# Performance work log

Hardware: AMD Instinct MI355X
Metric: run time of the kernel (lower is better)

The kernel has to match this reference:

```python
import jax, jax.numpy as jnp
import numpy as np

Nx, Nu, Ny, Np, H = 2, 1, 2, 8, 32
Nz = Np * (Nx + Nu)  # 24
B, T = 4096, 256
F, V, Delta = 0.1, 1.0, 1.0  # ps.squeeze(), volume, sample time
ymean = jnp.array([0.5, 0.5], jnp.float32)
ystd = jnp.array([0.3, 0.2], jnp.float32)
umean = jnp.array([1.0], jnp.float32)
ustd = jnp.array([0.5], jnp.float32)


def fnn(x, params):
    # dense layers: tanh hidden, linear output
    for W, b in params[:-1]:
        x = jnp.tanh(x @ W + b)
    W, b = params[-1]
    return x @ W + b


def fxzu(x, z, u, p1, p2, p3):
    # dCa/dt = F*(Caf-Ca)/V - r1 ; dCb/dt = -F*Cb/V + r1 - 3*r2 + r3
    Castd, Cbstd = ystd[0:1], ystd[1:2]
    r1 = fnn(x[:, 0:1], p1) * Castd
    r2 = fnn(x[:, 1:2], p2) * Cbstd
    r3 = fnn(z, p3) * Cbstd
    xs = x * ystd + ymean
    us = u * ustd + umean
    Ca, Cb, Caf = xs[:, 0:1], xs[:, 1:2], us[:, 0:1]
    dCa = F * (Caf - Ca) / V - r1
    dCb = -F * Cb / V + r1 - 3.0 * r2 + r3
    return jnp.concatenate([dCa, dCb], axis=-1) / ystd


def interp(yseq):
    # (B,(Np+1)*Nx) -> (B, Np*Nx): midpoints of consecutive Nx-blocks
    b = yseq.shape[0]
    y = yseq.reshape(b, Np + 1, Nx)
    return (0.5 * (y[:, :-1] + y[:, 1:])).reshape(b, Np * Nx)


def run(useq, xz0, p1, p2, p3):
    def step(xz, u):
        x, z = xz[:, :Nx], xz[:, Nx:]
        xpseq, upseq = z[:, :Np * Nx], z[:, Np * Nx:]
        k1 = fxzu(x, z, u, p1, p2, p3)
        z23 = jnp.concatenate([interp(jnp.concatenate([xpseq, x], -1)), upseq], -1)
        k2 = fxzu(x + Delta * k1 / 2, z23, u, p1, p2, p3)
        k3 = fxzu(x + Delta * k2 / 2, z23, u, p1, p2, p3)
        z4 = jnp.concatenate([xpseq[:, Nx:], x, upseq], -1)
        k4 = fxzu(x + Delta * k3, z4, u, p1, p2, p3)
        xplus = x + (Delta / 6.0) * (k1 + 2 * k2 + 2 * k3 + k4)
        zplus = jnp.concatenate([xpseq[:, Nx:], x, upseq[:, Nu:], u], -1)
        return jnp.concatenate([xplus, zplus], -1), x  # output is pre-update x
    _, ys = jax.lax.scan(step, xz0, jnp.swapaxes(useq, 0, 1))
    return jnp.swapaxes(ys, 0, 1)  # (B, T, Ny)


def setup_inputs() -> dict:
    key = jax.random.key(0)
    ks = jax.random.split(key, 12)
    inp = {
        'useq': jax.random.normal(ks[0], (B, T, Nu), jnp.float32),
        'xz0': jax.random.normal(ks[1], (B, Nx + Nz), jnp.float32),
    }
    dims = {'r1': [1, H, H, 1], 'r2': [1, H, H, 1], 'r3': [Nz, H, H, 1]}
    i = 2
    for name, ds in dims.items():
        for l, (din, dout) in enumerate(zip(ds[:-1], ds[1:])):
            inp[f'{name}W{l}'] = jax.random.normal(ks[i], (din, dout), jnp.float32) / np.sqrt(din).astype(np.float32)
            inp[f'{name}b{l}'] = jnp.zeros((dout,), jnp.float32)
            i += 1
    return inp


def reference(useq, xz0, r1W0, r1b0, r1W1, r1b1, r1W2, r1b2,
              r2W0, r2b0, r2W1, r2b1, r2W2, r2b2,
              r3W0, r3b0, r3W1, r3b1, r3W2, r3b2):
    p1 = [(r1W0, r1b0), (r1W1, r1b1), (r1W2, r1b2)]
    p2 = [(r2W0, r2b0), (r2W1, r2b1), (r2W2, r2b2)]
    p3 = [(r3W0, r3b0), (r3W1, r3b1), (r3W2, r3b2)]
    return run(useq, xz0, p1, p2, p3)
```

## Files before the change

kernel.cpp:

```cpp
#include <hip/hip_runtime.h>

#define DEVINL static __device__ __forceinline__
#define CFENCE() asm volatile("" ::: "memory")
#define PIN(x) asm volatile("" : "+v"(x))

typedef float v2f __attribute__((ext_vector_type(2)));

DEVINL v2f mk2(float a, float b) { v2f r; r.x = a; r.y = b; return r; }
DEVINL v2f pkfma(v2f a, v2f b, v2f c) { return __builtin_elementwise_fma(a, b, c); }

constexpr float KE = 2.885390081777927f;

#if __has_builtin(__builtin_amdgcn_exp2f)
DEVINL float exp2_fast(float x) { return __builtin_amdgcn_exp2f(x); }
#else
DEVINL float exp2_fast(float x) { return __expf(x * 0.6931471805599453f); }
#endif

DEVINL float tanh_pre(float t) {
  float e = exp2_fast(t);
  return 1.0f - 2.0f * __builtin_amdgcn_rcpf(e + 1.0f);
}

template <int CTRL>
DEVINL float dpp_add(float v) {
  int t = __builtin_amdgcn_update_dpp(0, __float_as_int(v), CTRL, 0xF, 0xF, true);
  return v + __int_as_float(t);
}
DEVINL float halves_psum(float v) {
  v = dpp_add<0xB1>(v);
  v = dpp_add<0x4E>(v);
  v = dpp_add<0x141>(v);
  v = dpp_add<0x140>(v);
  return v;
}
DEVINL float rlane(float v, int l) {
  return __int_as_float(__builtin_amdgcn_readlane(__float_as_int(v), l));
}

DEVINL float dot32(const float* hrow, const v2f* W, float bias) {
  const float4* hp = (const float4*)hrow;
  v2f a0 = mk2(bias, 0.f), a1 = mk2(0.f, 0.f);
  v2f a2 = mk2(0.f, 0.f), a3 = mk2(0.f, 0.f);
#pragma unroll
  for (int q = 0; q < 8; q += 2) {
    float4 x = hp[q], y = hp[q + 1];
    a0 = pkfma(mk2(x.x, x.y), W[2 * q + 0], a0);
    a1 = pkfma(mk2(x.z, x.w), W[2 * q + 1], a1);
    a2 = pkfma(mk2(y.x, y.y), W[2 * q + 2], a2);
    a3 = pkfma(mk2(y.z, y.w), W[2 * q + 3], a3);
  }
  v2f s = (a0 + a1) + (a2 + a3);
  return s.x + s.y;
}
DEVINL float pdot16(const float* hrow, const v2f* W) {
  const float4* hp = (const float4*)hrow;
  v2f a0 = mk2(0.f, 0.f), a1 = mk2(0.f, 0.f);
  float4 x = hp[0], y = hp[1];
  a0 = pkfma(mk2(x.x, x.y), W[0], a0);
  a1 = pkfma(mk2(x.z, x.w), W[1], a1);
  a0 = pkfma(mk2(y.x, y.y), W[2], a0);
  a1 = pkfma(mk2(y.z, y.w), W[3], a1);
  x = hp[2]; y = hp[3];
  a0 = pkfma(mk2(x.x, x.y), W[4], a0);
  a1 = pkfma(mk2(x.z, x.w), W[5], a1);
  a0 = pkfma(mk2(y.x, y.y), W[6], a0);
  a1 = pkfma(mk2(y.z, y.w), W[7], a1);
  v2f s = a0 + a1;
  return s.x + s.y;
}

constexpr int TT = 256;

__global__ __attribute__((amdgpu_flat_work_group_size(64, 64)))
__attribute__((amdgpu_waves_per_eu(4, 4))) void reac_kernel(
    const float* __restrict__ useq,
    const float* __restrict__ xz0,
    const float* __restrict__ r1W0, const float* __restrict__ r1b0,
    const float* __restrict__ r1W1, const float* __restrict__ r1b1,
    const float* __restrict__ r1W2, const float* __restrict__ r1b2,
    const float* __restrict__ r2W0, const float* __restrict__ r2b0,
    const float* __restrict__ r2W1, const float* __restrict__ r2b1,
    const float* __restrict__ r2W2, const float* __restrict__ r2b2,
    const float* __restrict__ r3W0, const float* __restrict__ r3b0,
    const float* __restrict__ r3W1, const float* __restrict__ r3b1,
    const float* __restrict__ r3W2, const float* __restrict__ r3b2,
    float2* __restrict__ out)
{
  const int lane = threadIdx.x;
  const int j = lane & 31;
  const bool hi = lane >= 32;
  const int b = blockIdx.x;
  const int xaddr = ((lane ^ 32) << 2);

  auto xchg = [&](float v) -> float {
    return __int_as_float(__builtin_amdgcn_ds_bpermute(xaddr, __float_as_int(v)));
  };

  const float* W0p = hi ? r2W0 : r1W0;
  const float* B0p = hi ? r2b0 : r1b0;
  const float* W1p = hi ? r2W1 : r1W1;
  const float* B1p = hi ? r2b1 : r1b1;
  const float* W2p = hi ? r2W2 : r1W2;
  const float sc = hi ? 0.2f : 0.3f;
  float w0K = W0p[j] * KE, b0K = B0p[j] * KE;
  float b1K = B1p[j] * KE;
  float w2sc = W2p[j] * sc;

  v2f W1v[16];
#pragma unroll
  for (int k = 0; k < 16; ++k)
    W1v[k] = mk2(W1p[(2 * k) * 32 + j] * KE, W1p[(2 * k + 1) * 32 + j] * KE);

  v2f W0Cv[12];
#pragma unroll
  for (int m = 0; m < 12; ++m) {
    int r = (hi && m >= 1 && m <= 7) ? (2 * m - 2) : (2 * m);
    v2f w = mk2(r3W0[r * 32 + j] * KE, r3W0[(r + 1) * 32 + j] * KE);
    if (hi && m == 0) w = mk2(0.f, 0.f);
    W0Cv[m] = w;
  }
  v2f WXv = mk2(r3W0[14 * 32 + j] * KE, r3W0[15 * 32 + j] * KE);

  const int kbase = hi ? 16 : 0;
  v2f W1Cv[8];
#pragma unroll
  for (int k = 0; k < 8; ++k)
    W1Cv[k] = mk2(r3W1[(kbase + 2 * k) * 32 + j] * KE,
                  r3W1[(kbase + 2 * k + 1) * 32 + j] * KE);
  float b0CK = r3b0[j] * KE, b1CK = r3b1[j] * KE;
  float w2C02 = r3W2[j] * 0.2f;

  PIN(w0K); PIN(b0K); PIN(b1K); PIN(w2sc);
  PIN(b0CK); PIN(b1CK); PIN(w2C02); PIN(WXv);
#pragma unroll
  for (int k = 0; k < 16; ++k) PIN(W1v[k]);
#pragma unroll
  for (int m = 0; m < 12; ++m) PIN(W0Cv[m]);
#pragma unroll
  for (int k = 0; k < 8; ++k) PIN(W1Cv[k]);

  const float b2sA = r1b2[0] * 0.3f;
  const float b2sB = r2b2[0] * 0.2f;
  const float b2Cs = r3b2[0] * 0.2f - 0.05f;

  __shared__ __align__(16) float zs[24];
  __shared__ __align__(16) float h12[2][32];
  __shared__ __align__(16) float hR3[3][32];

  float x0 = xz0[b * 26 + 0];
  float x1 = xz0[b * 26 + 1];
  if (!hi && j < 24) zs[j] = xz0[b * 26 + 2 + j];
  CFENCE();

  auto r3_l0 = [&](v2f& aaO, v2f& abO) {
    const float4* zp4 = (const float4*)&zs[0];
    float4 z0v = zp4[0], z1v = zp4[1], z2v = zp4[2], z3v = zp4[3];
    float4 u0v = zp4[4], u1v = zp4[5];
    v2f aa = mk2(b0CK, 0.f), ab = mk2(0.f, 0.f);
    aa = pkfma(mk2(z0v.x, z0v.y), W0Cv[0], aa);
    ab = pkfma(mk2(z0v.z, z0v.w), W0Cv[1], ab);
    aa = pkfma(mk2(z1v.x, z1v.y), W0Cv[2], aa);
    ab = pkfma(mk2(z1v.z, z1v.w), W0Cv[3], ab);
    aa = pkfma(mk2(z2v.x, z2v.y), W0Cv[4], aa);
    ab = pkfma(mk2(z2v.z, z2v.w), W0Cv[5], ab);
    aa = pkfma(mk2(z3v.x, z3v.y), W0Cv[6], aa);
    ab = pkfma(mk2(z3v.z, z3v.w), W0Cv[7], ab);
    aa = pkfma(mk2(u0v.x, u0v.y), W0Cv[8], aa);
    ab = pkfma(mk2(u0v.z, u0v.w), W0Cv[9], ab);
    aa = pkfma(mk2(u1v.x, u1v.y), W0Cv[10], aa);
    ab = pkfma(mk2(u1v.z, u1v.w), W0Cv[11], ab);
    aaO = aa; abO = ab;
  };
  auto rc1_eval = [&]() -> float {
    float p0 = pdot16(&hR3[0][kbase], W1Cv);
    float o0 = p0 + xchg(p0) + b1CK;
    float v = halves_psum(tanh_pre(o0) * w2C02);
    return (rlane(v, 15) + rlane(v, 31)) + b2Cs;
  };

  auto net_pre = [&](float sxv, float syv) -> float {
    float sv = hi ? syv : sxv;
    return tanh_pre(fmaf(sv, w0K, b0K));
  };
  auto net_post = [&](float sxv, float syv, float rc_m05, float CafF,
                      float& kx, float& ky) {
    float a = dot32(&h12[hi][0], W1v, b1K);
    float v = halves_psum(tanh_pre(a) * w2sc);
    float ra = (rlane(v, 15) + rlane(v, 31)) + b2sA;
    float rb = (rlane(v, 47) + rlane(v, 63)) + b2sB;
    float dCa = fmaf(-0.03f, sxv, CafF) - ra;
    float dCb = fmaf(-0.02f, syv, fmaf(-3.0f, rb, ra) + rc_m05);
    kx = dCa * (1.0f / 0.3f);
    ky = dCb * (1.0f / 0.2f);
  };

  v2f aa4, ab4;
  float Az;
  r3_l0(aa4, ab4);
  {
    v2f s = aa4 + ab4;
    Az = s.x + s.y;
    float h0 = tanh_pre(Az);
    CFENCE();
    if (!hi) hR3[0][j] = h0;
    CFENCE();
  }
  float rc1 = rc1_eval();

  float u = useq[b * TT];

  for (int t = 0; t < TT; ++t) {
    int tn = (t < TT - 1) ? (t + 1) : t;
    float u_nxt = useq[b * TT + tn];
    float CafF = fmaf(u, 0.05f, 0.05f);

    if (lane == 0) out[b * TT + t] = make_float2(x0, x1);

    ab4 = pkfma(mk2(x0, x1), WXv, ab4);
    v2f s4v = aa4 + ab4;
    float A4 = s4v.x + s4v.y;
    float Apart = xchg(hi ? A4 : Az);
    float targ = hi ? A4 : (0.5f * (Az + Apart));
    float hh = tanh_pre(targ);
    float h1 = net_pre(x0, x1);
    CFENCE();
    hR3[1 + hi][j] = hh;
    h12[hi][j] = h1;
    CFENCE();
    float p1 = pdot16(&hR3[1][kbase], W1Cv);
    float p2 = pdot16(&hR3[2][kbase], W1Cv);
    float o1 = p1 + xchg(p1) + b1CK;
    float o2 = p2 + xchg(p2) + b1CK;
    float vv = halves_psum(tanh_pre(hi ? o2 : o1) * w2C02);
    float rc23 = (rlane(vv, 15) + rlane(vv, 31)) + b2Cs;
    float rc4  = (rlane(vv, 47) + rlane(vv, 63)) + b2Cs;
    float kx1, ky1;
    net_post(x0, x1, rc1, CafF, kx1, ky1);
    float sx2 = fmaf(kx1, 0.5f, x0), sy2 = fmaf(ky1, 0.5f, x1);
    float h2 = net_pre(sx2, sy2);
    CFENCE();
    h12[hi][j] = h2;
    CFENCE();
    float kx2, ky2;
    net_post(sx2, sy2, rc23, CafF, kx2, ky2);
    {
      int src = (j < 14) ? (j + 2) : ((j < 23) ? (j + 1) : 0);
      float zread = zs[src];
      float znew = (j == 14) ? x0 : ((j == 15) ? x1 : ((j == 23) ? u : zread));
      if ((!hi) && (j < 24)) zs[j] = znew;
    }
    CFENCE();
    r3_l0(aa4, ab4);
    {
      v2f sv2 = aa4 + ab4;
      Az = sv2.x + sv2.y;
      float h0n = tanh_pre(Az);
      if (!hi) hR3[0][j] = h0n;
    }
    float sx3 = fmaf(kx2, 0.5f, x0), sy3 = fmaf(ky2, 0.5f, x1);
    float h3 = net_pre(sx3, sy3);
    CFENCE();
    h12[hi][j] = h3;
    CFENCE();
    float kx3, ky3;
    net_post(sx3, sy3, rc23, CafF, kx3, ky3);
    rc1 = rc1_eval();
    float sx4 = x0 + kx3, sy4 = x1 + ky3;
    float h4 = net_pre(sx4, sy4);
    CFENCE();
    h12[hi][j] = h4;
    CFENCE();
    float kx4, ky4;
    net_post(sx4, sy4, rc4, CafF, kx4, ky4);
    x0 += (kx1 + 2.0f * (kx2 + kx3) + kx4) * (1.0f / 6.0f);
    x1 += (ky1 + 2.0f * (ky2 + ky3) + ky4) * (1.0f / 6.0f);
    u = u_nxt;
    CFENCE();
  }
}

extern "C" void kernel_launch(void* const* d_in, const int* in_sizes, int n_in,
                              void* d_out, int out_size, void* d_ws, size_t ws_size,
                              hipStream_t stream) {
  const float* p[20];
  for (int i = 0; i < 20; ++i) p[i] = (const float*)d_in[i];
  reac_kernel<<<dim3(4096), dim3(64), 0, stream>>>(
      p[0], p[1], p[2], p[3], p[4], p[5], p[6], p[7], p[8], p[9], p[10],
      p[11], p[12], p[13], p[14], p[15], p[16], p[17], p[18], p[19],
      (float2*)d_out);
}
```

Before: 844.7 us.

## Move per-lane weights from registers to shared LDS and pack four waves per block

Per-lane weight vectors for the hidden layers used to be pinned in VGPRs. They now live in a shared-memory table written once by the first wave and read by all four waves of a 256-thread block, so each block handles four batch elements. The aim is to cut register pressure and the redundant weight loads so more waves fit per SIMD, which should hide the latency of this serial scan loop. The cost is extra LDS reads on every dot product inside the time loop, which may contend with the existing LDS traffic for activations.

```diff
diff --git a/kernel.cpp b/kernel.cpp
--- a/kernel.cpp
+++ b/kernel.cpp
@@ -2,7 +2,6 @@
 
 #define DEVINL static __device__ __forceinline__
 #define CFENCE() asm volatile("" ::: "memory")
-#define PIN(x) asm volatile("" : "+v"(x))
 
 typedef float v2f __attribute__((ext_vector_type(2)));
 
@@ -27,53 +26,20 @@
   int t = __builtin_amdgcn_update_dpp(0, __float_as_int(v), CTRL, 0xF, 0xF, true);
   return v + __int_as_float(t);
 }
-DEVINL float halves_psum(float v) {
+DEVINL float rlane(float v, int l) {
+  return __int_as_float(__builtin_amdgcn_readlane(__float_as_int(v), l));
+}
+DEVINL float psum4(float v) {
   v = dpp_add<0xB1>(v);
   v = dpp_add<0x4E>(v);
   v = dpp_add<0x141>(v);
   v = dpp_add<0x140>(v);
   return v;
 }
-DEVINL float rlane(float v, int l) {
-  return __int_as_float(__builtin_amdgcn_readlane(__float_as_int(v), l));
-}
-
-DEVINL float dot32(const float* hrow, const v2f* W, float bias) {
-  const float4* hp = (const float4*)hrow;
-  v2f a0 = mk2(bias, 0.f), a1 = mk2(0.f, 0.f);
-  v2f a2 = mk2(0.f, 0.f), a3 = mk2(0.f, 0.f);
-#pragma unroll
-  for (int q = 0; q < 8; q += 2) {
-    float4 x = hp[q], y = hp[q + 1];
-    a0 = pkfma(mk2(x.x, x.y), W[2 * q + 0], a0);
-    a1 = pkfma(mk2(x.z, x.w), W[2 * q + 1], a1);
-    a2 = pkfma(mk2(y.x, y.y), W[2 * q + 2], a2);
-    a3 = pkfma(mk2(y.z, y.w), W[2 * q + 3], a3);
-  }
-  v2f s = (a0 + a1) + (a2 + a3);
-  return s.x + s.y;
-}
-DEVINL float pdot16(const float* hrow, const v2f* W) {
-  const float4* hp = (const float4*)hrow;
-  v2f a0 = mk2(0.f, 0.f), a1 = mk2(0.f, 0.f);
-  float4 x = hp[0], y = hp[1];
-  a0 = pkfma(mk2(x.x, x.y), W[0], a0);
-  a1 = pkfma(mk2(x.z, x.w), W[1], a1);
-  a0 = pkfma(mk2(y.x, y.y), W[2], a0);
-  a1 = pkfma(mk2(y.z, y.w), W[3], a1);
-  x = hp[2]; y = hp[3];
-  a0 = pkfma(mk2(x.x, x.y), W[4], a0);
-  a1 = pkfma(mk2(x.z, x.w), W[5], a1);
-  a0 = pkfma(mk2(y.x, y.y), W[6], a0);
-  a1 = pkfma(mk2(y.z, y.w), W[7], a1);
-  v2f s = a0 + a1;
-  return s.x + s.y;
-}
 
 constexpr int TT = 256;
 
-__global__ __attribute__((amdgpu_flat_work_group_size(64, 64)))
-__attribute__((amdgpu_waves_per_eu(4, 4))) void reac_kernel(
+__global__ __attribute__((amdgpu_flat_work_group_size(256, 256))) void reac_kernel(
     const float* __restrict__ useq,
     const float* __restrict__ xz0,
     const float* __restrict__ r1W0, const float* __restrict__ r1b0,
@@ -87,106 +53,125 @@
     const float* __restrict__ r3W2, const float* __restrict__ r3b2,
     float2* __restrict__ out)
 {
-  const int lane = threadIdx.x;
-  const int j = lane & 31;
-  const bool hi = lane >= 32;
-  const int b = blockIdx.x;
-  const int xaddr = ((lane ^ 32) << 2);
+  const int tid = threadIdx.x;
+  const int w = tid >> 6;
+  const int ln = tid & 63;
+  const int j = ln & 31;
+  const bool hi = ln >= 32;
+  const int ge = blockIdx.x * 4 + w;
+  const int xaddr = ((ln ^ 32) << 2);
 
   auto xchg = [&](float v) -> float {
     return __int_as_float(__builtin_amdgcn_ds_bpermute(xaddr, __float_as_int(v)));
   };
 
-  const float* W0p = hi ? r2W0 : r1W0;
+  __shared__ __align__(16) v2f WT[37][64];
+  __shared__ __align__(16) float priv[4][192];
+  float* zs  = &priv[w][0];
+  float* h12 = &priv[w][32];
+  float* hR3 = &priv[w][96];
+
   const float* B0p = hi ? r2b0 : r1b0;
-  const float* W1p = hi ? r2W1 : r1W1;
   const float* B1p = hi ? r2b1 : r1b1;
-  const float* W2p = hi ? r2W2 : r1W2;
-  const float sc = hi ? 0.2f : 0.3f;
-  float w0K = W0p[j] * KE, b0K = B0p[j] * KE;
+  float w0K = (hi ? r2W0 : r1W0)[j] * KE, b0K = B0p[j] * KE;
   float b1K = B1p[j] * KE;
-  float w2sc = W2p[j] * sc;
-
-  v2f W1v[16];
-#pragma unroll
-  for (int k = 0; k < 16; ++k)
-    W1v[k] = mk2(W1p[(2 * k) * 32 + j] * KE, W1p[(2 * k + 1) * 32 + j] * KE);
-
-  v2f W0Cv[12];
-#pragma unroll
-  for (int m = 0; m < 12; ++m) {
-    int r = (hi && m >= 1 && m <= 7) ? (2 * m - 2) : (2 * m);
-    v2f w = mk2(r3W0[r * 32 + j] * KE, r3W0[(r + 1) * 32 + j] * KE);
-    if (hi && m == 0) w = mk2(0.f, 0.f);
-    W0Cv[m] = w;
-  }
-  v2f WXv = mk2(r3W0[14 * 32 + j] * KE, r3W0[15 * 32 + j] * KE);
-
-  const int kbase = hi ? 16 : 0;
-  v2f W1Cv[8];
-#pragma unroll
-  for (int k = 0; k < 8; ++k)
-    W1Cv[k] = mk2(r3W1[(kbase + 2 * k) * 32 + j] * KE,
-                  r3W1[(kbase + 2 * k + 1) * 32 + j] * KE);
+  float w2sc = (hi ? r2W2 : r1W2)[j] * (hi ? 0.2f : 0.3f);
   float b0CK = r3b0[j] * KE, b1CK = r3b1[j] * KE;
   float w2C02 = r3W2[j] * 0.2f;
-
-  PIN(w0K); PIN(b0K); PIN(b1K); PIN(w2sc);
-  PIN(b0CK); PIN(b1CK); PIN(w2C02); PIN(WXv);
-#pragma unroll
-  for (int k = 0; k < 16; ++k) PIN(W1v[k]);
-#pragma unroll
-  for (int m = 0; m < 12; ++m) PIN(W0Cv[m]);
-#pragma unroll
-  for (int k = 0; k < 8; ++k) PIN(W1Cv[k]);
-
   const float b2sA = r1b2[0] * 0.3f;
   const float b2sB = r2b2[0] * 0.2f;
   const float b2Cs = r3b2[0] * 0.2f - 0.05f;
-
-  __shared__ __align__(16) float zs[24];
-  __shared__ __align__(16) float h12[2][32];
-  __shared__ __align__(16) float hR3[3][32];
-
-  float x0 = xz0[b * 26 + 0];
-  float x1 = xz0[b * 26 + 1];
-  if (!hi && j < 24) zs[j] = xz0[b * 26 + 2 + j];
-  CFENCE();
-
+  const int kbase = hi ? 16 : 0;
+
+  if (tid < 64) {
+    const float* W1p = hi ? r2W1 : r1W1;
+#pragma unroll
+    for (int k = 0; k < 16; ++k)
+      WT[k][ln] = mk2(W1p[(2 * k) * 32 + j] * KE,
+                      W1p[(2 * k + 1) * 32 + j] * KE);
+#pragma unroll
+    for (int m = 0; m < 12; ++m) {
+      int r = (hi && m >= 1 && m <= 7) ? (2 * m - 2) : (2 * m);
+      v2f wv = mk2(r3W0[r * 32 + j] * KE, r3W0[(r + 1) * 32 + j] * KE);
+      if (hi && m == 0) wv = mk2(0.f, 0.f);
+      WT[16 + m][ln] = wv;
+    }
+#pragma unroll
+    for (int k = 0; k < 8; ++k)
+      WT[28 + k][ln] = mk2(r3W1[(kbase + 2 * k) * 32 + j] * KE,
+                           r3W1[(kbase + 2 * k + 1) * 32 + j] * KE);
+    WT[36][ln] = mk2(r3W0[14 * 32 + j] * KE, r3W0[15 * 32 + j] * KE);
+  }
+
+  float x0 = xz0[ge * 26 + 0];
+  float x1 = xz0[ge * 26 + 1];
+  if (!hi && j < 24) zs[j] = xz0[ge * 26 + 2 + j];
+  __syncthreads();
+
+  auto dot32W = [&](const float* hrow, float bias) -> float {
+    const float4* hp = (const float4*)hrow;
+    v2f a0 = mk2(bias, 0.f), a1 = mk2(0.f, 0.f);
+    v2f a2 = mk2(0.f, 0.f), a3 = mk2(0.f, 0.f);
+#pragma unroll
+    for (int q = 0; q < 8; q += 2) {
+      float4 x = hp[q], y = hp[q + 1];
+      a0 = pkfma(mk2(x.x, x.y), WT[2 * q + 0][ln], a0);
+      a1 = pkfma(mk2(x.z, x.w), WT[2 * q + 1][ln], a1);
+      a2 = pkfma(mk2(y.x, y.y), WT[2 * q + 2][ln], a2);
+      a3 = pkfma(mk2(y.z, y.w), WT[2 * q + 3][ln], a3);
+    }
+    v2f s = (a0 + a1) + (a2 + a3);
+    return s.x + s.y;
+  };
+  auto pdot16W = [&](const float* hrow) -> float {
+    const float4* hp = (const float4*)hrow;
+    v2f a0 = mk2(0.f, 0.f), a1 = mk2(0.f, 0.f);
+    float4 x = hp[0], y = hp[1];
+    a0 = pkfma(mk2(x.x, x.y), WT[28][ln], a0);
+    a1 = pkfma(mk2(x.z, x.w), WT[29][ln], a1);
+    a0 = pkfma(mk2(y.x, y.y), WT[30][ln], a0);
+    a1 = pkfma(mk2(y.z, y.w), WT[31][ln], a1);
+    x = hp[2]; y = hp[3];
+    a0 = pkfma(mk2(x.x, x.y), WT[32][ln], a0);
+    a1 = pkfma(mk2(x.z, x.w), WT[33][ln], a1);
+    a0 = pkfma(mk2(y.x, y.y), WT[34][ln], a0);
+    a1 = pkfma(mk2(y.z, y.w), WT[35][ln], a1);
+    v2f s = a0 + a1;
+    return s.x + s.y;
+  };
   auto r3_l0 = [&](v2f& aaO, v2f& abO) {
-    const float4* zp4 = (const float4*)&zs[0];
-    float4 z0v = zp4[0], z1v = zp4[1], z2v = zp4[2], z3v = zp4[3];
-    float4 u0v = zp4[4], u1v = zp4[5];
+    const float4* zp = (const float4*)zs;
+    float4 z0 = zp[0], z1 = zp[1], z2 = zp[2], z3 = zp[3];
+    float4 u0 = zp[4], u1 = zp[5];
     v2f aa = mk2(b0CK, 0.f), ab = mk2(0.f, 0.f);
-    aa = pkfma(mk2(z0v.x, z0v.y), W0Cv[0], aa);
-    ab = pkfma(mk2(z0v.z, z0v.w), W0Cv[1], ab);
-    aa = pkfma(mk2(z1v.x, z1v.y), W0Cv[2], aa);
-    ab = pkfma(mk2(z1v.z, z1v.w), W0Cv[3], ab);
-    aa = pkfma(mk2(z2v.x, z2v.y), W0Cv[4], aa);
-    ab = pkfma(mk2(z2v.z, z2v.w), W0Cv[5], ab);
-    aa = pkfma(mk2(z3v.x, z3v.y), W0Cv[6], aa);
-    ab = pkfma(mk2(z3v.z, z3v.w), W0Cv[7], ab);
-    aa = pkfma(mk2(u0v.x, u0v.y), W0Cv[8], aa);
-    ab = pkfma(mk2(u0v.z, u0v.w), W0Cv[9], ab);
-    aa = pkfma(mk2(u1v.x, u1v.y), W0Cv[10], aa);
-    ab = pkfma(mk2(u1v.z, u1v.w), W0Cv[11], ab);
+    aa = pkfma(mk2(z0.x, z0.y), WT[16][ln], aa);
+    ab = pkfma(mk2(z0.z, z0.w), WT[17][ln], ab);
+    aa = pkfma(mk2(z1.x, z1.y), WT[18][ln], aa);
+    ab = pkfma(mk2(z1.z, z1.w), WT[19][ln], ab);
+    aa = pkfma(mk2(z2.x, z2.y), WT[20][ln], aa);
+    ab = pkfma(mk2(z2.z, z2.w), WT[21][ln], ab);
+    aa = pkfma(mk2(z3.x, z3.y), WT[22][ln], aa);
+    ab = pkfma(mk2(z3.z, z3.w), WT[23][ln], ab);
+    aa = pkfma(mk2(u0.x, u0.y), WT[24][ln], aa);
+    ab = pkfma(mk2(u0.z, u0.w), WT[25][ln], ab);
+    aa = pkfma(mk2(u1.x, u1.y), WT[26][ln], aa);
+    ab = pkfma(mk2(u1.z, u1.w), WT[27][ln], ab);
     aaO = aa; abO = ab;
   };
   auto rc1_eval = [&]() -> float {
-    float p0 = pdot16(&hR3[0][kbase], W1Cv);
+    float p0 = pdot16W(&hR3[kbase]);
     float o0 = p0 + xchg(p0) + b1CK;
-    float v = halves_psum(tanh_pre(o0) * w2C02);
+    float v = psum4(tanh_pre(o0) * w2C02);
     return (rlane(v, 15) + rlane(v, 31)) + b2Cs;
   };
-
   auto net_pre = [&](float sxv, float syv) -> float {
     float sv = hi ? syv : sxv;
     return tanh_pre(fmaf(sv, w0K, b0K));
   };
   auto net_post = [&](float sxv, float syv, float rc_m05, float CafF,
                       float& kx, float& ky) {
-    float a = dot32(&h12[hi][0], W1v, b1K);
-    float v = halves_psum(tanh_pre(a) * w2sc);
+    float a = dot32W(&h12[hi ? 32 : 0], b1K);
+    float v = psum4(tanh_pre(a) * w2sc);
     float ra = (rlane(v, 15) + rlane(v, 31)) + b2sA;
     float rb = (rlane(v, 47) + rlane(v, 63)) + b2sB;
     float dCa = fmaf(-0.03f, sxv, CafF) - ra;
@@ -203,21 +188,23 @@
     Az = s.x + s.y;
     float h0 = tanh_pre(Az);
     CFENCE();
-    if (!hi) hR3[0][j] = h0;
+    if (!hi) hR3[j] = h0;
     CFENCE();
   }
   float rc1 = rc1_eval();
 
-  float u = useq[b * TT];
+  const float* up = useq + ge * TT;
+  float2* outp = out + ge * TT;
+  float u = up[0];
 
   for (int t = 0; t < TT; ++t) {
     int tn = (t < TT - 1) ? (t + 1) : t;
-    float u_nxt = useq[b * TT + tn];
+    float u_nxt = up[tn];
     float CafF = fmaf(u, 0.05f, 0.05f);
 
-    if (lane == 0) out[b * TT + t] = make_float2(x0, x1);
-
-    ab4 = pkfma(mk2(x0, x1), WXv, ab4);
+    if (ln == 0) outp[t] = make_float2(x0, x1);
+
+    ab4 = pkfma(mk2(x0, x1), WT[36][ln], ab4);
     v2f s4v = aa4 + ab4;
     float A4 = s4v.x + s4v.y;
     float Apart = xchg(hi ? A4 : Az);
@@ -225,14 +212,14 @@
     float hh = tanh_pre(targ);
     float h1 = net_pre(x0, x1);
     CFENCE();
-    hR3[1 + hi][j] = hh;
-    h12[hi][j] = h1;
-    CFENCE();
-    float p1 = pdot16(&hR3[1][kbase], W1Cv);
-    float p2 = pdot16(&hR3[2][kbase], W1Cv);
+    hR3[32 * (1 + (hi ? 1 : 0)) + j] = hh;
+    h12[(hi ? 32 : 0) + j] = h1;
+    CFENCE();
+    float p1 = pdot16W(&hR3[32 + kbase]);
+    float p2 = pdot16W(&hR3[64 + kbase]);
     float o1 = p1 + xchg(p1) + b1CK;
     float o2 = p2 + xchg(p2) + b1CK;
-    float vv = halves_psum(tanh_pre(hi ? o2 : o1) * w2C02);
+    float vv = psum4(tanh_pre(hi ? o2 : o1) * w2C02);
     float rc23 = (rlane(vv, 15) + rlane(vv, 31)) + b2Cs;
     float rc4  = (rlane(vv, 47) + rlane(vv, 63)) + b2Cs;
     float kx1, ky1;
@@ -240,7 +227,7 @@
     float sx2 = fmaf(kx1, 0.5f, x0), sy2 = fmaf(ky1, 0.5f, x1);
     float h2 = net_pre(sx2, sy2);
     CFENCE();
-    h12[hi][j] = h2;
+    h12[(hi ? 32 : 0) + j] = h2;
     CFENCE();
     float kx2, ky2;
     net_post(sx2, sy2, rc23, CafF, kx2, ky2);
@@ -256,12 +243,12 @@
       v2f sv2 = aa4 + ab4;
       Az = sv2.x + sv2.y;
       float h0n = tanh_pre(Az);
-      if (!hi) hR3[0][j] = h0n;
+      if (!hi) hR3[j] = h0n;
     }
     float sx3 = fmaf(kx2, 0.5f, x0), sy3 = fmaf(ky2, 0.5f, x1);
     float h3 = net_pre(sx3, sy3);
     CFENCE();
-    h12[hi][j] = h3;
+    h12[(hi ? 32 : 0) + j] = h3;
     CFENCE();
     float kx3, ky3;
     net_post(sx3, sy3, rc23, CafF, kx3, ky3);
@@ -269,7 +256,7 @@
     float sx4 = x0 + kx3, sy4 = x1 + ky3;
     float h4 = net_pre(sx4, sy4);
     CFENCE();
-    h12[hi][j] = h4;
+    h12[(hi ? 32 : 0) + j] = h4;
     CFENCE();
     float kx4, ky4;
     net_post(sx4, sy4, rc4, CafF, kx4, ky4);
@@ -285,7 +272,7 @@
                               hipStream_t stream) {
   const float* p[20];
   for (int i = 0; i < 20; ++i) p[i] = (const float*)d_in[i];
-  reac_kernel<<<dim3(4096), dim3(64), 0, stream>>>(
+  reac_kernel<<<dim3(1024), dim3(256), 0, stream>>>(
       p[0], p[1], p[2], p[3], p[4], p[5], p[6], p[7], p[8], p[9], p[10],
       p[11], p[12], p[13], p[14], p[15], p[16], p[17], p[18], p[19],
       (float2*)d_out);
```

Result: slower. 1.339 ms (+58.5%).

## Double-buffer z history in LDS and hoist next-step r3 layer-0 earlier

Applied to the files above, without the earlier changes.

Splits the z history into two shared buffers so the shifted next-step z can be written early, alongside the stage-1 hidden values, instead of in a separate fenced block. The next step's r3 first layer and the rc1 evaluation move earlier in the RK4 stages, overlapping with the r1/r2 stage work. Also removes the register-pinning asm on the weight vectors, which lets the compiler schedule them freely but may raise register pressure or cause rematerialisation. Each step now keeps more values live across stages, and correctness relies on the pointer swap at the end of every iteration.

```diff
diff --git a/kernel.cpp b/kernel.cpp
--- a/kernel.cpp
+++ b/kernel.cpp
@@ -2,7 +2,6 @@
 
 #define DEVINL static __device__ __forceinline__
 #define CFENCE() asm volatile("" ::: "memory")
-#define PIN(x) asm volatile("" : "+v"(x))
 
 typedef float v2f __attribute__((ext_vector_type(2)));
 
@@ -27,15 +26,15 @@
   int t = __builtin_amdgcn_update_dpp(0, __float_as_int(v), CTRL, 0xF, 0xF, true);
   return v + __int_as_float(t);
 }
-DEVINL float halves_psum(float v) {
+DEVINL float rlane(float v, int l) {
+  return __int_as_float(__builtin_amdgcn_readlane(__float_as_int(v), l));
+}
+DEVINL float psum4(float v) {
   v = dpp_add<0xB1>(v);
   v = dpp_add<0x4E>(v);
   v = dpp_add<0x141>(v);
   v = dpp_add<0x140>(v);
   return v;
-}
-DEVINL float rlane(float v, int l) {
-  return __int_as_float(__builtin_amdgcn_readlane(__float_as_int(v), l));
 }
 
 DEVINL float dot32(const float* hrow, const v2f* W, float bias) {
@@ -131,54 +130,47 @@
   float b0CK = r3b0[j] * KE, b1CK = r3b1[j] * KE;
   float w2C02 = r3W2[j] * 0.2f;
 
-  PIN(w0K); PIN(b0K); PIN(b1K); PIN(w2sc);
-  PIN(b0CK); PIN(b1CK); PIN(w2C02); PIN(WXv);
-#pragma unroll
-  for (int k = 0; k < 16; ++k) PIN(W1v[k]);
-#pragma unroll
-  for (int m = 0; m < 12; ++m) PIN(W0Cv[m]);
-#pragma unroll
-  for (int k = 0; k < 8; ++k) PIN(W1Cv[k]);
-
   const float b2sA = r1b2[0] * 0.3f;
   const float b2sB = r2b2[0] * 0.2f;
   const float b2Cs = r3b2[0] * 0.2f - 0.05f;
 
-  __shared__ __align__(16) float zs[24];
+  __shared__ __align__(16) float zs2[2][24];
   __shared__ __align__(16) float h12[2][32];
   __shared__ __align__(16) float hR3[3][32];
 
+  float* zsC = &zs2[0][0];
+  float* zsN = &zs2[1][0];
+
   float x0 = xz0[b * 26 + 0];
   float x1 = xz0[b * 26 + 1];
-  if (!hi && j < 24) zs[j] = xz0[b * 26 + 2 + j];
+  if (!hi && j < 24) zsC[j] = xz0[b * 26 + 2 + j];
   CFENCE();
 
-  auto r3_l0 = [&](v2f& aaO, v2f& abO) {
-    const float4* zp4 = (const float4*)&zs[0];
-    float4 z0v = zp4[0], z1v = zp4[1], z2v = zp4[2], z3v = zp4[3];
-    float4 u0v = zp4[4], u1v = zp4[5];
+  auto r3_l0 = [&](const float* zp_, v2f& aaO, v2f& abO) {
+    const float4* zp = (const float4*)zp_;
+    float4 z0 = zp[0], z1 = zp[1], z2 = zp[2], z3 = zp[3];
+    float4 u0 = zp[4], u1 = zp[5];
     v2f aa = mk2(b0CK, 0.f), ab = mk2(0.f, 0.f);
-    aa = pkfma(mk2(z0v.x, z0v.y), W0Cv[0], aa);
-    ab = pkfma(mk2(z0v.z, z0v.w), W0Cv[1], ab);
-    aa = pkfma(mk2(z1v.x, z1v.y), W0Cv[2], aa);
-    ab = pkfma(mk2(z1v.z, z1v.w), W0Cv[3], ab);
-    aa = pkfma(mk2(z2v.x, z2v.y), W0Cv[4], aa);
-    ab = pkfma(mk2(z2v.z, z2v.w), W0Cv[5], ab);
-    aa = pkfma(mk2(z3v.x, z3v.y), W0Cv[6], aa);
-    ab = pkfma(mk2(z3v.z, z3v.w), W0Cv[7], ab);
-    aa = pkfma(mk2(u0v.x, u0v.y), W0Cv[8], aa);
-    ab = pkfma(mk2(u0v.z, u0v.w), W0Cv[9], ab);
-    aa = pkfma(mk2(u1v.x, u1v.y), W0Cv[10], aa);
-    ab = pkfma(mk2(u1v.z, u1v.w), W0Cv[11], ab);
+    aa = pkfma(mk2(z0.x, z0.y), W0Cv[0], aa);
+    ab = pkfma(mk2(z0.z, z0.w), W0Cv[1], ab);
+    aa = pkfma(mk2(z1.x, z1.y), W0Cv[2], aa);
+    ab = pkfma(mk2(z1.z, z1.w), W0Cv[3], ab);
+    aa = pkfma(mk2(z2.x, z2.y), W0Cv[4], aa);
+    ab = pkfma(mk2(z2.z, z2.w), W0Cv[5], ab);
+    aa = pkfma(mk2(z3.x, z3.y), W0Cv[6], aa);
+    ab = pkfma(mk2(z3.z, z3.w), W0Cv[7], ab);
+    aa = pkfma(mk2(u0.x, u0.y), W0Cv[8], aa);
+    ab = pkfma(mk2(u0.z, u0.w), W0Cv[9], ab);
+    aa = pkfma(mk2(u1.x, u1.y), W0Cv[10], aa);
+    ab = pkfma(mk2(u1.z, u1.w), W0Cv[11], ab);
     aaO = aa; abO = ab;
   };
   auto rc1_eval = [&]() -> float {
     float p0 = pdot16(&hR3[0][kbase], W1Cv);
     float o0 = p0 + xchg(p0) + b1CK;
-    float v = halves_psum(tanh_pre(o0) * w2C02);
+    float v = psum4(tanh_pre(o0) * w2C02);
     return (rlane(v, 15) + rlane(v, 31)) + b2Cs;
   };
-
   auto net_pre = [&](float sxv, float syv) -> float {
     float sv = hi ? syv : sxv;
     return tanh_pre(fmaf(sv, w0K, b0K));
@@ -186,7 +178,7 @@
   auto net_post = [&](float sxv, float syv, float rc_m05, float CafF,
                       float& kx, float& ky) {
     float a = dot32(&h12[hi][0], W1v, b1K);
-    float v = halves_psum(tanh_pre(a) * w2sc);
+    float v = psum4(tanh_pre(a) * w2sc);
     float ra = (rlane(v, 15) + rlane(v, 31)) + b2sA;
     float rb = (rlane(v, 47) + rlane(v, 63)) + b2sB;
     float dCa = fmaf(-0.03f, sxv, CafF) - ra;
@@ -197,7 +189,7 @@
 
   v2f aa4, ab4;
   float Az;
-  r3_l0(aa4, ab4);
+  r3_l0(zsC, aa4, ab4);
   {
     v2f s = aa4 + ab4;
     Az = s.x + s.y;
@@ -224,40 +216,36 @@
     float targ = hi ? A4 : (0.5f * (Az + Apart));
     float hh = tanh_pre(targ);
     float h1 = net_pre(x0, x1);
+    int src = (j < 14) ? (j + 2) : ((j < 23) ? (j + 1) : 0);
+    float zread = zsC[src];
+    float znew = (j == 14) ? x0 : ((j == 15) ? x1 : ((j == 23) ? u : zread));
     CFENCE();
     hR3[1 + hi][j] = hh;
     h12[hi][j] = h1;
+    if (!hi && j < 24) zsN[j] = znew;
     CFENCE();
     float p1 = pdot16(&hR3[1][kbase], W1Cv);
     float p2 = pdot16(&hR3[2][kbase], W1Cv);
     float o1 = p1 + xchg(p1) + b1CK;
     float o2 = p2 + xchg(p2) + b1CK;
-    float vv = halves_psum(tanh_pre(hi ? o2 : o1) * w2C02);
+    float vv = psum4(tanh_pre(hi ? o2 : o1) * w2C02);
     float rc23 = (rlane(vv, 15) + rlane(vv, 31)) + b2Cs;
     float rc4  = (rlane(vv, 47) + rlane(vv, 63)) + b2Cs;
     float kx1, ky1;
     net_post(x0, x1, rc1, CafF, kx1, ky1);
+    r3_l0(zsN, aa4, ab4);
+    v2f sv2 = aa4 + ab4;
+    Az = sv2.x + sv2.y;
+    float h0n = tanh_pre(Az);
     float sx2 = fmaf(kx1, 0.5f, x0), sy2 = fmaf(ky1, 0.5f, x1);
     float h2 = net_pre(sx2, sy2);
     CFENCE();
     h12[hi][j] = h2;
+    if (!hi) hR3[0][j] = h0n;
     CFENCE();
     float kx2, ky2;
     net_post(sx2, sy2, rc23, CafF, kx2, ky2);
-    {
-      int src = (j < 14) ? (j + 2) : ((j < 23) ? (j + 1) : 0);
-      float zread = zs[src];
-      float znew = (j == 14) ? x0 : ((j == 15) ? x1 : ((j == 23) ? u : zread));
-      if ((!hi) && (j < 24)) zs[j] = znew;
-    }
-    CFENCE();
-    r3_l0(aa4, ab4);
-    {
-      v2f sv2 = aa4 + ab4;
-      Az = sv2.x + sv2.y;
-      float h0n = tanh_pre(Az);
-      if (!hi) hR3[0][j] = h0n;
-    }
+    rc1 = rc1_eval();
     float sx3 = fmaf(kx2, 0.5f, x0), sy3 = fmaf(ky2, 0.5f, x1);
     float h3 = net_pre(sx3, sy3);
     CFENCE();
@@ -265,7 +253,6 @@
     CFENCE();
     float kx3, ky3;
     net_post(sx3, sy3, rc23, CafF, kx3, ky3);
-    rc1 = rc1_eval();
     float sx4 = x0 + kx3, sy4 = x1 + ky3;
     float h4 = net_pre(sx4, sy4);
     CFENCE();
@@ -276,6 +263,7 @@
     x0 += (kx1 + 2.0f * (kx2 + kx3) + kx4) * (1.0f / 6.0f);
     x1 += (ky1 + 2.0f * (ky2 + ky3) + ky4) * (1.0f / 6.0f);
     u = u_nxt;
+    float* ztmp = zsC; zsC = zsN; zsN = ztmp;
     CFENCE();
   }
 }
```

New measurement: 843.5 us. About the same (-0.1%).
